# Performance work log

Hardware: AMD Instinct MI355X
Metric: run time of the kernel (lower is better)

Reference implementation:

```python
import jax, jax.numpy as jnp
import numpy as np

DIM, N_HEAD, DK, DV = 1024, 16, 64, 64
B, S = 1, 4096


def setup_inputs() -> dict:
    key = jax.random.key(0)
    ks = jax.random.split(key, 9)
    sd = 0.02
    return {
        "x": jax.random.normal(ks[0], (B, S, DIM), dtype=jnp.float32),
        "Wq": jax.random.normal(ks[1], (DIM, N_HEAD * DK), dtype=jnp.float32) * sd,
        "bq": jnp.zeros((N_HEAD * DK,), dtype=jnp.float32),
        "Wk": jax.random.normal(ks[2], (DIM, N_HEAD * DK), dtype=jnp.float32) * sd,
        "bk": jnp.zeros((N_HEAD * DK,), dtype=jnp.float32),
        "Wv": jax.random.normal(ks[3], (DIM, N_HEAD * DV), dtype=jnp.float32) * sd,
        "bv": jnp.zeros((N_HEAD * DV,), dtype=jnp.float32),
        "Wo": jax.random.normal(ks[4], (N_HEAD * DV, DIM), dtype=jnp.float32) * sd,
        "bo": jnp.zeros((DIM,), dtype=jnp.float32),
    }


def reference(x, Wq, bq, Wk, bk, Wv, bv, Wo, bo):
    b, s, _ = x.shape
    scale = DK ** (-0.5)
    # projections -> [b, h, s, d]
    q = (x @ Wq + bq).reshape(b, s, N_HEAD, DK).transpose(0, 2, 1, 3)
    k = (x @ Wk + bk).reshape(b, s, N_HEAD, DK).transpose(0, 2, 1, 3)
    v = (x @ Wv + bv).reshape(b, s, N_HEAD, DV).transpose(0, 2, 1, 3)
    attn = jnp.einsum("bhqd,bhkd->bhqk", q, k) * scale  # [b,h,s,s]
    attn = jax.nn.softmax(attn, axis=-1)
    out = jnp.einsum("bhqk,bhkd->bhqd", attn, v)  # [b,h,s,dv]
    out = out.transpose(0, 2, 1, 3).reshape(b, s, N_HEAD * DV)
    return out @ Wo + bo
```

## Files before the change

kernel.cpp:

```cpp
#include <hip/hip_runtime.h>
#include <hip/hip_bf16.h>
#include <hip/hip_fp16.h>

#define SEQ 4096
#define DIM 1024
#define NH 16
#define NT (SEQ / 64)

typedef __attribute__((ext_vector_type(4))) float f32x4;
typedef __attribute__((ext_vector_type(16))) float f32x16;
typedef __attribute__((ext_vector_type(8))) _Float16 half8;
typedef __attribute__((ext_vector_type(4))) _Float16 half4;

typedef const unsigned __attribute__((address_space(1)))* gas_t;
typedef unsigned __attribute__((address_space(3)))* las_t;

#if __has_builtin(__builtin_amdgcn_exp2f)
#define EXP2(x) __builtin_amdgcn_exp2f(x)
#else
#define EXP2(x) exp2f(x)
#endif

#define SMC 0.18033688f

__global__ __launch_bounds__(256) void prep_all(const float* __restrict__ x,
                                                _Float16* __restrict__ xh,
                                                const float* __restrict__ W0,
                                                const float* __restrict__ W1,
                                                const float* __restrict__ W2,
                                                const float* __restrict__ W3,
                                                _Float16* __restrict__ T0,
                                                _Float16* __restrict__ T1,
                                                _Float16* __restrict__ T2,
                                                _Float16* __restrict__ T3) {
  if (blockIdx.z == 4) {
    const int blkid = blockIdx.x * 32 + blockIdx.y;
#pragma unroll
    for (int u = 0; u < 4; u++) {
      int i = blkid * 4096 + u * 1024 + threadIdx.x * 4;
      float4 v = *reinterpret_cast<const float4*>(x + i);
      half4 h;
      h[0] = (_Float16)v.x; h[1] = (_Float16)v.y;
      h[2] = (_Float16)v.z; h[3] = (_Float16)v.w;
      *reinterpret_cast<half4*>(xh + i) = h;
    }
    return;
  }
  const float* W = blockIdx.z == 0 ? W0 : blockIdx.z == 1 ? W1 : blockIdx.z == 2 ? W2 : W3;
  _Float16* Wt = blockIdx.z == 0 ? T0 : blockIdx.z == 1 ? T1 : blockIdx.z == 2 ? T2 : T3;
  __shared__ float t[32][33];
  int bx = blockIdx.x * 32;
  int by = blockIdx.y * 32;
  int tx = threadIdx.x & 31, ty = threadIdx.x >> 5;
#pragma unroll
  for (int i = 0; i < 4; i++)
    t[ty + i * 8][tx] = W[(by + ty + i * 8) * DIM + bx + tx];
  __syncthreads();
#pragma unroll
  for (int i = 0; i < 4; i++)
    Wt[(bx + ty + i * 8) * DIM + by + tx] = (_Float16)t[tx][ty + i * 8];
}

template <int MODE>
__device__ __forceinline__ void gemm_body(const _Float16* __restrict__ A,
                                          const _Float16* __restrict__ Bt,
                                          const float* __restrict__ bias,
                                          void* __restrict__ outp,
                                          int M, int N, int Kd, int bmb, int bnb) {
  __shared__ __align__(16) _Float16 As[128][32];
  __shared__ __align__(16) _Float16 Bs[128][32];
  const int tid = threadIdx.x, lane = tid & 63, w = tid >> 6;
  const int bm = bmb * 128, bn = bnb * 128;
  const int l15 = lane & 15, g = lane >> 4, kb = g * 8;
  const int wr = (w >> 1) * 64, wc = (w & 1) * 64;
  const int lr = lane >> 2;
  const int lc = (lane & 3) * 8;
  f32x4 acc[4][4] = {};

  for (int k0 = 0; k0 < Kd; k0 += 32) {
    __syncthreads();
    const _Float16* as0 = A + (size_t)(bm + w * 32 + lr) * Kd + k0 + lc;
    __builtin_amdgcn_global_load_lds((gas_t)(const void*)as0,
                                     (las_t)(void*)&As[w * 32][0], 16, 0, 0);
    __builtin_amdgcn_global_load_lds((gas_t)(const void*)(as0 + (size_t)16 * Kd),
                                     (las_t)(void*)&As[w * 32 + 16][0], 16, 0, 0);
    const _Float16* bs0 = Bt + (size_t)(bn + w * 32 + lr) * Kd + k0 + lc;
    __builtin_amdgcn_global_load_lds((gas_t)(const void*)bs0,
                                     (las_t)(void*)&Bs[w * 32][0], 16, 0, 0);
    __builtin_amdgcn_global_load_lds((gas_t)(const void*)(bs0 + (size_t)16 * Kd),
                                     (las_t)(void*)&Bs[w * 32 + 16][0], 16, 0, 0);
    __syncthreads();

    half8 af[4], bf[4];
#pragma unroll
    for (int i = 0; i < 4; i++)
      af[i] = *reinterpret_cast<const half8*>(&As[wr + i * 16 + l15][kb]);
#pragma unroll
    for (int j = 0; j < 4; j++)
      bf[j] = *reinterpret_cast<const half8*>(&Bs[wc + j * 16 + l15][kb]);
    __builtin_amdgcn_s_setprio(1);
#pragma unroll
    for (int i = 0; i < 4; i++)
#pragma unroll
      for (int j = 0; j < 4; j++)
        acc[i][j] = __builtin_amdgcn_mfma_f32_16x16x32_f16(af[i], bf[j], acc[i][j], 0, 0, 0);
    __builtin_amdgcn_s_setprio(0);
  }

  const int gswap = ((g & 1) << 1) | (g >> 1);
#pragma unroll
  for (int i = 0; i < 4; i++)
#pragma unroll
    for (int j = 0; j < 4; j++) {
      const int col = bn + wc + j * 16 + l15;
      if (MODE == 2) {
        const int rowP = bm + wr + i * 16 + gswap * 4;
        half4 hv;
#pragma unroll
        for (int r = 0; r < 4; r++) hv[r] = (_Float16)(acc[i][j][r] + bias[col]);
        *reinterpret_cast<half4*>(&((_Float16*)outp)[(size_t)col * M + rowP]) = hv;
      } else {
        const int row0 = bm + wr + i * 16 + g * 4;
#pragma unroll
        for (int r = 0; r < 4; r++) {
          float vv = acc[i][j][r] + bias[col];
          if (MODE == 0) {
            _Float16* O = (_Float16*)outp;
            O[(((col >> 6) * SEQ) + row0 + r) * 64 + (col & 63)] = (_Float16)vv;
          } else {
            float* O = (float*)outp;
            O[(size_t)(row0 + r) * N + col] = vv;
          }
        }
      }
    }
}

__global__ __launch_bounds__(256) void gemm_qkv(const _Float16* __restrict__ A,
                                                const _Float16* __restrict__ WqT,
                                                const _Float16* __restrict__ WkT,
                                                const _Float16* __restrict__ WvT,
                                                const float* __restrict__ bq,
                                                const float* __restrict__ bk,
                                                const float* __restrict__ bv,
                                                _Float16* __restrict__ Qd,
                                                _Float16* __restrict__ Kd,
                                                _Float16* __restrict__ Vd) {
  if (blockIdx.z == 0)
    gemm_body<0>(A, WqT, bq, (void*)Qd, SEQ, DIM, DIM, blockIdx.x, blockIdx.y);
  else if (blockIdx.z == 1)
    gemm_body<0>(A, WkT, bk, (void*)Kd, SEQ, DIM, DIM, blockIdx.x, blockIdx.y);
  else
    gemm_body<2>(A, WvT, bv, (void*)Vd, SEQ, DIM, DIM, blockIdx.x, blockIdx.y);
}

__global__ __launch_bounds__(256) void gemm_out(const _Float16* __restrict__ A,
                                                const _Float16* __restrict__ Bt,
                                                const float* __restrict__ bias,
                                                float* __restrict__ out) {
  gemm_body<1>(A, Bt, bias, (void*)out, SEQ, DIM, DIM, blockIdx.x, blockIdx.y);
}

__global__ __launch_bounds__(512) void attn_fwd(const _Float16* __restrict__ Q,
                                                const _Float16* __restrict__ Kh,
                                                const _Float16* __restrict__ Vt_g,
                                                _Float16* __restrict__ Og) {
  __shared__ __align__(16) _Float16 Ks[3][64][72];
  __shared__ __align__(16) _Float16 Vs[3][64][72];
  const int hh = blockIdx.y;
  const int q0 = blockIdx.x * 256;
  const int tid = threadIdx.x, lane = tid & 63, w = tid >> 6;
  const int l31 = lane & 31, hq = lane >> 5, h8 = hq * 8;

  const int qrow = q0 + w * 32 + l31;
  const _Float16* qp = Q + ((size_t)hh * SEQ + qrow) * 64;
  half8 qf[4];
#pragma unroll
  for (int d = 0; d < 4; d++)
    qf[d] = *reinterpret_cast<const half8*>(qp + d * 16 + h8);

  f32x16 o[2] = {};
  float m = -1e30f, lsum = 0.f, negmC = 1e30f;
  const f32x16 kZero16 = {};

  const int srow = tid >> 3, sc8 = (tid & 7) * 8;
  const _Float16* kbase = Kh + (size_t)hh * SEQ * 64;
  const _Float16* vbase = Vt_g + (size_t)hh * 64 * SEQ;

  uint4 kr, vr;
  auto LOADKV = [&](int kt2) {
    kr = *reinterpret_cast<const uint4*>(kbase + (size_t)(kt2 * 64 + srow) * 64 + sc8);
    vr = *reinterpret_cast<const uint4*>(vbase + (size_t)srow * SEQ + kt2 * 64 + sc8);
  };
  auto STAGE = [&](int buf) {
    *reinterpret_cast<uint4*>(&Ks[buf][srow][sc8]) = kr;
    *reinterpret_cast<uint4*>(&Vs[buf][srow][sc8]) = vr;
  };

  auto QK = [&](int tile, f32x16 (&sf)[2]) {
    const int b = tile % 3;
    __builtin_amdgcn_s_setprio(1);
    {
      half8 kf0 = *reinterpret_cast<const half8*>(&Ks[b][l31][h8]);
      half8 kf1 = *reinterpret_cast<const half8*>(&Ks[b][32 + l31][h8]);
      sf[0] = __builtin_amdgcn_mfma_f32_32x32x16_f16(kf0, qf[0], kZero16, 0, 0, 0);
      sf[1] = __builtin_amdgcn_mfma_f32_32x32x16_f16(kf1, qf[0], kZero16, 0, 0, 0);
    }
#pragma unroll
    for (int d = 1; d < 4; d++) {
      half8 kf0 = *reinterpret_cast<const half8*>(&Ks[b][l31][d * 16 + h8]);
      half8 kf1 = *reinterpret_cast<const half8*>(&Ks[b][32 + l31][d * 16 + h8]);
      sf[0] = __builtin_amdgcn_mfma_f32_32x32x16_f16(kf0, qf[d], sf[0], 0, 0, 0);
      sf[1] = __builtin_amdgcn_mfma_f32_32x32x16_f16(kf1, qf[d], sf[1], 0, 0, 0);
    }
    __builtin_amdgcn_s_setprio(0);
  };

  auto ITER = [&](int t, f32x16 (&scur)[2], f32x16 (&snext)[2]) {
    if (t + 1 < NT) QK(t + 1, snext);
    if (t + 2 < NT) STAGE((t + 2) % 3);
    if (t + 3 < NT) LOADKV(t + 3);

    float t0 = fmaxf(fmaxf(scur[0][0], scur[0][1]), scur[0][2]);
    float t1 = fmaxf(fmaxf(scur[0][3], scur[0][4]), scur[0][5]);
    float t2 = fmaxf(fmaxf(scur[0][6], scur[0][7]), scur[0][8]);
    float t3 = fmaxf(fmaxf(scur[0][9], scur[0][10]), scur[0][11]);
    float t4 = fmaxf(fmaxf(scur[0][12], scur[0][13]), scur[0][14]);
    float t5 = fmaxf(fmaxf(scur[0][15], scur[1][0]), scur[1][1]);
    float t6 = fmaxf(fmaxf(scur[1][2], scur[1][3]), scur[1][4]);
    float t7 = fmaxf(fmaxf(scur[1][5], scur[1][6]), scur[1][7]);
    float t8 = fmaxf(fmaxf(scur[1][8], scur[1][9]), scur[1][10]);
    float t9 = fmaxf(fmaxf(scur[1][11], scur[1][12]), scur[1][13]);
    float ta = fmaxf(scur[1][14], scur[1][15]);
    float u0 = fmaxf(fmaxf(t0, t1), t2);
    float u1 = fmaxf(fmaxf(t3, t4), t5);
    float u2 = fmaxf(fmaxf(t6, t7), t8);
    float u3 = fmaxf(t9, ta);
    float pm = fmaxf(fmaxf(fmaxf(u0, u1), u2), u3);

    if (__any(pm > m + 64.f)) {
      pm = fmaxf(pm, __shfl_xor(pm, 32, 64));
      float mn = fmaxf(m, pm);
      float al = EXP2((m - mn) * SMC);
      m = mn;
      negmC = -mn * SMC;
      lsum *= al;
      o[0] *= al;
      o[1] *= al;
    }
    f32x16 pf0, pf1;
    float s0 = 0.f, s1 = 0.f, s2 = 0.f, s3 = 0.f;
#pragma unroll
    for (int r = 0; r < 16; r += 4) {
      float p0 = EXP2(fmaf(scur[0][r + 0], SMC, negmC));
      float p1 = EXP2(fmaf(scur[0][r + 1], SMC, negmC));
      float p2 = EXP2(fmaf(scur[0][r + 2], SMC, negmC));
      float p3 = EXP2(fmaf(scur[0][r + 3], SMC, negmC));
      pf0[r + 0] = p0; pf0[r + 1] = p1; pf0[r + 2] = p2; pf0[r + 3] = p3;
      s0 += p0; s1 += p1; s2 += p2; s3 += p3;
    }
#pragma unroll
    for (int r = 0; r < 16; r += 4) {
      float p0 = EXP2(fmaf(scur[1][r + 0], SMC, negmC));
      float p1 = EXP2(fmaf(scur[1][r + 1], SMC, negmC));
      float p2 = EXP2(fmaf(scur[1][r + 2], SMC, negmC));
      float p3 = EXP2(fmaf(scur[1][r + 3], SMC, negmC));
      pf1[r + 0] = p0; pf1[r + 1] = p1; pf1[r + 2] = p2; pf1[r + 3] = p3;
      s0 += p0; s1 += p1; s2 += p2; s3 += p3;
    }
    lsum += (s0 + s1) + (s2 + s3);

    half8 pb[4];
#pragma unroll
    for (int s = 0; s < 4; s++) {
      const int base = (s & 1) * 8;
      unsigned d0, d1, d2, d3;
      if (s < 2) {
        d0 = __builtin_bit_cast(unsigned, __builtin_amdgcn_cvt_pkrtz(pf0[base + 0], pf0[base + 1]));
        d1 = __builtin_bit_cast(unsigned, __builtin_amdgcn_cvt_pkrtz(pf0[base + 2], pf0[base + 3]));
        d2 = __builtin_bit_cast(unsigned, __builtin_amdgcn_cvt_pkrtz(pf0[base + 4], pf0[base + 5]));
        d3 = __builtin_bit_cast(unsigned, __builtin_amdgcn_cvt_pkrtz(pf0[base + 6], pf0[base + 7]));
      } else {
        d0 = __builtin_bit_cast(unsigned, __builtin_amdgcn_cvt_pkrtz(pf1[base + 0], pf1[base + 1]));
        d1 = __builtin_bit_cast(unsigned, __builtin_amdgcn_cvt_pkrtz(pf1[base + 2], pf1[base + 3]));
        d2 = __builtin_bit_cast(unsigned, __builtin_amdgcn_cvt_pkrtz(pf1[base + 4], pf1[base + 5]));
        d3 = __builtin_bit_cast(unsigned, __builtin_amdgcn_cvt_pkrtz(pf1[base + 6], pf1[base + 7]));
      }
      uint4 uu = {d0, d1, d2, d3};
      pb[s] = __builtin_bit_cast(half8, uu);
    }

    const int bv = t % 3;
    __builtin_amdgcn_s_setprio(1);
#pragma unroll
    for (int s = 0; s < 4; s++) {
      half8 va0 = *reinterpret_cast<const half8*>(&Vs[bv][l31][s * 16 + h8]);
      half8 va1 = *reinterpret_cast<const half8*>(&Vs[bv][32 + l31][s * 16 + h8]);
      o[0] = __builtin_amdgcn_mfma_f32_32x32x16_f16(va0, pb[s], o[0], 0, 0, 0);
      o[1] = __builtin_amdgcn_mfma_f32_32x32x16_f16(va1, pb[s], o[1], 0, 0, 0);
    }
    __builtin_amdgcn_s_setprio(0);

    __syncthreads();
  };

  LOADKV(0); STAGE(0);
  LOADKV(1); STAGE(1);
  LOADKV(2);
  __syncthreads();

  f32x16 sfA[2], sfB[2];
  QK(0, sfA);
  for (int t = 0; t < NT; t += 2) {
    ITER(t, sfA, sfB);
    ITER(t + 1, sfB, sfA);
  }

  float ls = lsum + __shfl_xor(lsum, 32, 64);
  float rinv = 1.f / ls;
#pragma unroll
  for (int tile = 0; tile < 2; tile++)
#pragma unroll
    for (int rg = 0; rg < 4; rg++) {
      half4 hv;
#pragma unroll
      for (int j = 0; j < 4; j++) hv[j] = (_Float16)(o[tile][rg * 4 + j] * rinv);
      const int dv = tile * 32 + rg * 8 + 4 * hq;
      *reinterpret_cast<half4*>(&Og[(size_t)qrow * DIM + hh * 64 + dv]) = hv;
    }
}


extern "C" void kernel_launch(void* const* d_in, const int* in_sizes, int n_in,
                              void* d_out, int out_size, void* d_ws, size_t ws_size,
                              hipStream_t stream) {
  const float* x  = (const float*)d_in[0];
  const float* Wq = (const float*)d_in[1];
  const float* bq = (const float*)d_in[2];
  const float* Wk = (const float*)d_in[3];
  const float* bk = (const float*)d_in[4];
  const float* Wv = (const float*)d_in[5];
  const float* bv = (const float*)d_in[6];
  const float* Wo = (const float*)d_in[7];
  const float* bo = (const float*)d_in[8];

  char* ws = (char*)d_ws;
  _Float16* xh  = (_Float16*)ws;
  _Float16* WqT = (_Float16*)(ws + (size_t)SEQ * DIM * 2);
  _Float16* WkT = WqT + DIM * DIM;
  _Float16* WvT = WkT + DIM * DIM;
  _Float16* WoT = WvT + DIM * DIM;
  _Float16* Qd  = WoT + DIM * DIM;
  _Float16* Kd  = Qd + (size_t)SEQ * DIM;
  _Float16* Vd  = Kd + (size_t)SEQ * DIM;
  _Float16* Od  = Vd + (size_t)SEQ * DIM;

  prep_all<<<dim3(32, 32, 5), 256, 0, stream>>>(x, xh, Wq, Wk, Wv, Wo,
                                                WqT, WkT, WvT, WoT);

  gemm_qkv<<<dim3(SEQ / 128, DIM / 128, 3), 256, 0, stream>>>(
      xh, WqT, WkT, WvT, bq, bk, bv, Qd, Kd, Vd);

  attn_fwd<<<dim3(SEQ / 256, NH), 512, 0, stream>>>(Qd, Kd, Vd, Od);

  gemm_out<<<dim3(SEQ / 128, DIM / 128), 256, 0, stream>>>(Od, WoT, bo, (float*)d_out);
}
```

Baseline: 162.9 us.

## Give each attention wave two 32-row query tiles, halve block threads

The attention kernel now runs 256 threads per block (4 waves), each wave handling 64 query rows as two 32-row sub-tiles that share the same K and V fragments read from LDS. Each thread loads twice as much K/V per stage to keep the 256-row block tile. This halves LDS fragment reads per unit of MFMA work and doubles independent MFMA chains per wave. The cost is roughly double the accumulator and score registers per thread, with launch_bounds(256,1) allowing more VGPRs but possibly lowering occupancy.

```diff
diff --git a/kernel.cpp b/kernel.cpp
--- a/kernel.cpp
+++ b/kernel.cpp
@@ -161,10 +161,10 @@
   gemm_body<1>(A, Bt, bias, (void*)out, SEQ, DIM, DIM, blockIdx.x, blockIdx.y);
 }
 
-__global__ __launch_bounds__(512) void attn_fwd(const _Float16* __restrict__ Q,
-                                                const _Float16* __restrict__ Kh,
-                                                const _Float16* __restrict__ Vt_g,
-                                                _Float16* __restrict__ Og) {
+__global__ __launch_bounds__(256, 1) void attn_fwd(const _Float16* __restrict__ Q,
+                                                   const _Float16* __restrict__ Kh,
+                                                   const _Float16* __restrict__ Vt_g,
+                                                   _Float16* __restrict__ Og) {
   __shared__ __align__(16) _Float16 Ks[3][64][72];
   __shared__ __align__(16) _Float16 Vs[3][64][72];
   const int hh = blockIdx.y;
@@ -172,122 +172,139 @@
   const int tid = threadIdx.x, lane = tid & 63, w = tid >> 6;
   const int l31 = lane & 31, hq = lane >> 5, h8 = hq * 8;
 
-  const int qrow = q0 + w * 32 + l31;
-  const _Float16* qp = Q + ((size_t)hh * SEQ + qrow) * 64;
-  half8 qf[4];
-#pragma unroll
-  for (int d = 0; d < 4; d++)
-    qf[d] = *reinterpret_cast<const half8*>(qp + d * 16 + h8);
-
-  f32x16 o[2] = {};
-  float m = -1e30f, lsum = 0.f, negmC = 1e30f;
+  const int qrow0 = q0 + w * 64 + l31;
+  const _Float16* qp0 = Q + ((size_t)hh * SEQ + qrow0) * 64;
+  half8 qf[2][4];
+#pragma unroll
+  for (int d = 0; d < 4; d++) {
+    qf[0][d] = *reinterpret_cast<const half8*>(qp0 + d * 16 + h8);
+    qf[1][d] = *reinterpret_cast<const half8*>(qp0 + 32 * 64 + d * 16 + h8);
+  }
+
+  f32x16 o[2][2] = {};
+  float m[2] = {-1e30f, -1e30f};
+  float lsum[2] = {0.f, 0.f};
+  float negmC[2] = {1e30f, 1e30f};
   const f32x16 kZero16 = {};
 
-  const int srow = tid >> 3, sc8 = (tid & 7) * 8;
+  const int srow = tid >> 2, scc = (tid & 3) * 16;
   const _Float16* kbase = Kh + (size_t)hh * SEQ * 64;
   const _Float16* vbase = Vt_g + (size_t)hh * 64 * SEQ;
 
-  uint4 kr, vr;
+  uint4 kr0, kr1, vr0, vr1;
   auto LOADKV = [&](int kt2) {
-    kr = *reinterpret_cast<const uint4*>(kbase + (size_t)(kt2 * 64 + srow) * 64 + sc8);
-    vr = *reinterpret_cast<const uint4*>(vbase + (size_t)srow * SEQ + kt2 * 64 + sc8);
+    const _Float16* kp = kbase + (size_t)(kt2 * 64 + srow) * 64 + scc;
+    kr0 = *reinterpret_cast<const uint4*>(kp);
+    kr1 = *reinterpret_cast<const uint4*>(kp + 8);
+    const _Float16* vp = vbase + (size_t)srow * SEQ + kt2 * 64 + scc;
+    vr0 = *reinterpret_cast<const uint4*>(vp);
+    vr1 = *reinterpret_cast<const uint4*>(vp + 8);
   };
   auto STAGE = [&](int buf) {
-    *reinterpret_cast<uint4*>(&Ks[buf][srow][sc8]) = kr;
-    *reinterpret_cast<uint4*>(&Vs[buf][srow][sc8]) = vr;
+    *reinterpret_cast<uint4*>(&Ks[buf][srow][scc]) = kr0;
+    *reinterpret_cast<uint4*>(&Ks[buf][srow][scc + 8]) = kr1;
+    *reinterpret_cast<uint4*>(&Vs[buf][srow][scc]) = vr0;
+    *reinterpret_cast<uint4*>(&Vs[buf][srow][scc + 8]) = vr1;
   };
 
-  auto QK = [&](int tile, f32x16 (&sf)[2]) {
+  auto QK = [&](int tile, f32x16 (&sf)[2][2]) {
     const int b = tile % 3;
     __builtin_amdgcn_s_setprio(1);
     {
       half8 kf0 = *reinterpret_cast<const half8*>(&Ks[b][l31][h8]);
       half8 kf1 = *reinterpret_cast<const half8*>(&Ks[b][32 + l31][h8]);
-      sf[0] = __builtin_amdgcn_mfma_f32_32x32x16_f16(kf0, qf[0], kZero16, 0, 0, 0);
-      sf[1] = __builtin_amdgcn_mfma_f32_32x32x16_f16(kf1, qf[0], kZero16, 0, 0, 0);
+      sf[0][0] = __builtin_amdgcn_mfma_f32_32x32x16_f16(kf0, qf[0][0], kZero16, 0, 0, 0);
+      sf[0][1] = __builtin_amdgcn_mfma_f32_32x32x16_f16(kf1, qf[0][0], kZero16, 0, 0, 0);
+      sf[1][0] = __builtin_amdgcn_mfma_f32_32x32x16_f16(kf0, qf[1][0], kZero16, 0, 0, 0);
+      sf[1][1] = __builtin_amdgcn_mfma_f32_32x32x16_f16(kf1, qf[1][0], kZero16, 0, 0, 0);
     }
 #pragma unroll
     for (int d = 1; d < 4; d++) {
       half8 kf0 = *reinterpret_cast<const half8*>(&Ks[b][l31][d * 16 + h8]);
       half8 kf1 = *reinterpret_cast<const half8*>(&Ks[b][32 + l31][d * 16 + h8]);
-      sf[0] = __builtin_amdgcn_mfma_f32_32x32x16_f16(kf0, qf[d], sf[0], 0, 0, 0);
-      sf[1] = __builtin_amdgcn_mfma_f32_32x32x16_f16(kf1, qf[d], sf[1], 0, 0, 0);
+      sf[0][0] = __builtin_amdgcn_mfma_f32_32x32x16_f16(kf0, qf[0][d], sf[0][0], 0, 0, 0);
+      sf[0][1] = __builtin_amdgcn_mfma_f32_32x32x16_f16(kf1, qf[0][d], sf[0][1], 0, 0, 0);
+      sf[1][0] = __builtin_amdgcn_mfma_f32_32x32x16_f16(kf0, qf[1][d], sf[1][0], 0, 0, 0);
+      sf[1][1] = __builtin_amdgcn_mfma_f32_32x32x16_f16(kf1, qf[1][d], sf[1][1], 0, 0, 0);
     }
     __builtin_amdgcn_s_setprio(0);
   };
 
-  auto ITER = [&](int t, f32x16 (&scur)[2], f32x16 (&snext)[2]) {
+  auto ITER = [&](int t, f32x16 (&scur)[2][2], f32x16 (&snext)[2][2]) {
     if (t + 1 < NT) QK(t + 1, snext);
     if (t + 2 < NT) STAGE((t + 2) % 3);
     if (t + 3 < NT) LOADKV(t + 3);
 
-    float t0 = fmaxf(fmaxf(scur[0][0], scur[0][1]), scur[0][2]);
-    float t1 = fmaxf(fmaxf(scur[0][3], scur[0][4]), scur[0][5]);
-    float t2 = fmaxf(fmaxf(scur[0][6], scur[0][7]), scur[0][8]);
-    float t3 = fmaxf(fmaxf(scur[0][9], scur[0][10]), scur[0][11]);
-    float t4 = fmaxf(fmaxf(scur[0][12], scur[0][13]), scur[0][14]);
-    float t5 = fmaxf(fmaxf(scur[0][15], scur[1][0]), scur[1][1]);
-    float t6 = fmaxf(fmaxf(scur[1][2], scur[1][3]), scur[1][4]);
-    float t7 = fmaxf(fmaxf(scur[1][5], scur[1][6]), scur[1][7]);
-    float t8 = fmaxf(fmaxf(scur[1][8], scur[1][9]), scur[1][10]);
-    float t9 = fmaxf(fmaxf(scur[1][11], scur[1][12]), scur[1][13]);
-    float ta = fmaxf(scur[1][14], scur[1][15]);
-    float u0 = fmaxf(fmaxf(t0, t1), t2);
-    float u1 = fmaxf(fmaxf(t3, t4), t5);
-    float u2 = fmaxf(fmaxf(t6, t7), t8);
-    float u3 = fmaxf(t9, ta);
-    float pm = fmaxf(fmaxf(fmaxf(u0, u1), u2), u3);
-
-    if (__any(pm > m + 64.f)) {
-      pm = fmaxf(pm, __shfl_xor(pm, 32, 64));
-      float mn = fmaxf(m, pm);
-      float al = EXP2((m - mn) * SMC);
-      m = mn;
-      negmC = -mn * SMC;
-      lsum *= al;
-      o[0] *= al;
-      o[1] *= al;
-    }
-    f32x16 pf0, pf1;
-    float s0 = 0.f, s1 = 0.f, s2 = 0.f, s3 = 0.f;
-#pragma unroll
-    for (int r = 0; r < 16; r += 4) {
-      float p0 = EXP2(fmaf(scur[0][r + 0], SMC, negmC));
-      float p1 = EXP2(fmaf(scur[0][r + 1], SMC, negmC));
-      float p2 = EXP2(fmaf(scur[0][r + 2], SMC, negmC));
-      float p3 = EXP2(fmaf(scur[0][r + 3], SMC, negmC));
-      pf0[r + 0] = p0; pf0[r + 1] = p1; pf0[r + 2] = p2; pf0[r + 3] = p3;
-      s0 += p0; s1 += p1; s2 += p2; s3 += p3;
-    }
-#pragma unroll
-    for (int r = 0; r < 16; r += 4) {
-      float p0 = EXP2(fmaf(scur[1][r + 0], SMC, negmC));
-      float p1 = EXP2(fmaf(scur[1][r + 1], SMC, negmC));
-      float p2 = EXP2(fmaf(scur[1][r + 2], SMC, negmC));
-      float p3 = EXP2(fmaf(scur[1][r + 3], SMC, negmC));
-      pf1[r + 0] = p0; pf1[r + 1] = p1; pf1[r + 2] = p2; pf1[r + 3] = p3;
-      s0 += p0; s1 += p1; s2 += p2; s3 += p3;
-    }
-    lsum += (s0 + s1) + (s2 + s3);
-
-    half8 pb[4];
-#pragma unroll
-    for (int s = 0; s < 4; s++) {
-      const int base = (s & 1) * 8;
-      unsigned d0, d1, d2, d3;
-      if (s < 2) {
-        d0 = __builtin_bit_cast(unsigned, __builtin_amdgcn_cvt_pkrtz(pf0[base + 0], pf0[base + 1]));
-        d1 = __builtin_bit_cast(unsigned, __builtin_amdgcn_cvt_pkrtz(pf0[base + 2], pf0[base + 3]));
-        d2 = __builtin_bit_cast(unsigned, __builtin_amdgcn_cvt_pkrtz(pf0[base + 4], pf0[base + 5]));
-        d3 = __builtin_bit_cast(unsigned, __builtin_amdgcn_cvt_pkrtz(pf0[base + 6], pf0[base + 7]));
-      } else {
-        d0 = __builtin_bit_cast(unsigned, __builtin_amdgcn_cvt_pkrtz(pf1[base + 0], pf1[base + 1]));
-        d1 = __builtin_bit_cast(unsigned, __builtin_amdgcn_cvt_pkrtz(pf1[base + 2], pf1[base + 3]));
-        d2 = __builtin_bit_cast(unsigned, __builtin_amdgcn_cvt_pkrtz(pf1[base + 4], pf1[base + 5]));
-        d3 = __builtin_bit_cast(unsigned, __builtin_amdgcn_cvt_pkrtz(pf1[base + 6], pf1[base + 7]));
-      }
-      uint4 uu = {d0, d1, d2, d3};
-      pb[s] = __builtin_bit_cast(half8, uu);
+    half8 pb[2][4];
+#pragma unroll
+    for (int qa = 0; qa < 2; qa++) {
+      float t0 = fmaxf(fmaxf(scur[qa][0][0], scur[qa][0][1]), scur[qa][0][2]);
+      float t1 = fmaxf(fmaxf(scur[qa][0][3], scur[qa][0][4]), scur[qa][0][5]);
+      float t2 = fmaxf(fmaxf(scur[qa][0][6], scur[qa][0][7]), scur[qa][0][8]);
+      float t3 = fmaxf(fmaxf(scur[qa][0][9], scur[qa][0][10]), scur[qa][0][11]);
+      float t4 = fmaxf(fmaxf(scur[qa][0][12], scur[qa][0][13]), scur[qa][0][14]);
+      float t5 = fmaxf(fmaxf(scur[qa][0][15], scur[qa][1][0]), scur[qa][1][1]);
+      float t6 = fmaxf(fmaxf(scur[qa][1][2], scur[qa][1][3]), scur[qa][1][4]);
+      float t7 = fmaxf(fmaxf(scur[qa][1][5], scur[qa][1][6]), scur[qa][1][7]);
+      float t8 = fmaxf(fmaxf(scur[qa][1][8], scur[qa][1][9]), scur[qa][1][10]);
+      float t9 = fmaxf(fmaxf(scur[qa][1][11], scur[qa][1][12]), scur[qa][1][13]);
+      float ta = fmaxf(scur[qa][1][14], scur[qa][1][15]);
+      float u0 = fmaxf(fmaxf(t0, t1), t2);
+      float u1 = fmaxf(fmaxf(t3, t4), t5);
+      float u2 = fmaxf(fmaxf(t6, t7), t8);
+      float u3 = fmaxf(t9, ta);
+      float pm = fmaxf(fmaxf(fmaxf(u0, u1), u2), u3);
+
+      if (__any(pm > m[qa] + 64.f)) {
+        pm = fmaxf(pm, __shfl_xor(pm, 32, 64));
+        float mn = fmaxf(m[qa], pm);
+        float al = EXP2((m[qa] - mn) * SMC);
+        m[qa] = mn;
+        negmC[qa] = -mn * SMC;
+        lsum[qa] *= al;
+        o[qa][0] *= al;
+        o[qa][1] *= al;
+      }
+      f32x16 pf0, pf1;
+      float s0 = 0.f, s1 = 0.f, s2 = 0.f, s3 = 0.f;
+#pragma unroll
+      for (int r = 0; r < 16; r += 4) {
+        float p0 = EXP2(fmaf(scur[qa][0][r + 0], SMC, negmC[qa]));
+        float p1 = EXP2(fmaf(scur[qa][0][r + 1], SMC, negmC[qa]));
+        float p2 = EXP2(fmaf(scur[qa][0][r + 2], SMC, negmC[qa]));
+        float p3 = EXP2(fmaf(scur[qa][0][r + 3], SMC, negmC[qa]));
+        pf0[r + 0] = p0; pf0[r + 1] = p1; pf0[r + 2] = p2; pf0[r + 3] = p3;
+        s0 += p0; s1 += p1; s2 += p2; s3 += p3;
+      }
+#pragma unroll
+      for (int r = 0; r < 16; r += 4) {
+        float p0 = EXP2(fmaf(scur[qa][1][r + 0], SMC, negmC[qa]));
+        float p1 = EXP2(fmaf(scur[qa][1][r + 1], SMC, negmC[qa]));
+        float p2 = EXP2(fmaf(scur[qa][1][r + 2], SMC, negmC[qa]));
+        float p3 = EXP2(fmaf(scur[qa][1][r + 3], SMC, negmC[qa]));
+        pf1[r + 0] = p0; pf1[r + 1] = p1; pf1[r + 2] = p2; pf1[r + 3] = p3;
+        s0 += p0; s1 += p1; s2 += p2; s3 += p3;
+      }
+      lsum[qa] += (s0 + s1) + (s2 + s3);
+
+#pragma unroll
+      for (int s = 0; s < 4; s++) {
+        const int base = (s & 1) * 8;
+        unsigned d0, d1, d2, d3;
+        if (s < 2) {
+          d0 = __builtin_bit_cast(unsigned, __builtin_amdgcn_cvt_pkrtz(pf0[base + 0], pf0[base + 1]));
+          d1 = __builtin_bit_cast(unsigned, __builtin_amdgcn_cvt_pkrtz(pf0[base + 2], pf0[base + 3]));
+          d2 = __builtin_bit_cast(unsigned, __builtin_amdgcn_cvt_pkrtz(pf0[base + 4], pf0[base + 5]));
+          d3 = __builtin_bit_cast(unsigned, __builtin_amdgcn_cvt_pkrtz(pf0[base + 6], pf0[base + 7]));
+        } else {
+          d0 = __builtin_bit_cast(unsigned, __builtin_amdgcn_cvt_pkrtz(pf1[base + 0], pf1[base + 1]));
+          d1 = __builtin_bit_cast(unsigned, __builtin_amdgcn_cvt_pkrtz(pf1[base + 2], pf1[base + 3]));
+          d2 = __builtin_bit_cast(unsigned, __builtin_amdgcn_cvt_pkrtz(pf1[base + 4], pf1[base + 5]));
+          d3 = __builtin_bit_cast(unsigned, __builtin_amdgcn_cvt_pkrtz(pf1[base + 6], pf1[base + 7]));
+        }
+        uint4 uu = {d0, d1, d2, d3};
+        pb[qa][s] = __builtin_bit_cast(half8, uu);
+      }
     }
 
     const int bv = t % 3;
@@ -296,8 +313,10 @@
     for (int s = 0; s < 4; s++) {
       half8 va0 = *reinterpret_cast<const half8*>(&Vs[bv][l31][s * 16 + h8]);
       half8 va1 = *reinterpret_cast<const half8*>(&Vs[bv][32 + l31][s * 16 + h8]);
-      o[0] = __builtin_amdgcn_mfma_f32_32x32x16_f16(va0, pb[s], o[0], 0, 0, 0);
-      o[1] = __builtin_amdgcn_mfma_f32_32x32x16_f16(va1, pb[s], o[1], 0, 0, 0);
+      o[0][0] = __builtin_amdgcn_mfma_f32_32x32x16_f16(va0, pb[0][s], o[0][0], 0, 0, 0);
+      o[0][1] = __builtin_amdgcn_mfma_f32_32x32x16_f16(va1, pb[0][s], o[0][1], 0, 0, 0);
+      o[1][0] = __builtin_amdgcn_mfma_f32_32x32x16_f16(va0, pb[1][s], o[1][0], 0, 0, 0);
+      o[1][1] = __builtin_amdgcn_mfma_f32_32x32x16_f16(va1, pb[1][s], o[1][1], 0, 0, 0);
     }
     __builtin_amdgcn_s_setprio(0);
 
@@ -309,25 +328,29 @@
   LOADKV(2);
   __syncthreads();
 
-  f32x16 sfA[2], sfB[2];
+  f32x16 sfA[2][2], sfB[2][2];
   QK(0, sfA);
   for (int t = 0; t < NT; t += 2) {
     ITER(t, sfA, sfB);
     ITER(t + 1, sfB, sfA);
   }
 
-  float ls = lsum + __shfl_xor(lsum, 32, 64);
-  float rinv = 1.f / ls;
-#pragma unroll
-  for (int tile = 0; tile < 2; tile++)
-#pragma unroll
-    for (int rg = 0; rg < 4; rg++) {
-      half4 hv;
-#pragma unroll
-      for (int j = 0; j < 4; j++) hv[j] = (_Float16)(o[tile][rg * 4 + j] * rinv);
-      const int dv = tile * 32 + rg * 8 + 4 * hq;
-      *reinterpret_cast<half4*>(&Og[(size_t)qrow * DIM + hh * 64 + dv]) = hv;
-    }
+#pragma unroll
+  for (int qa = 0; qa < 2; qa++) {
+    float ls = lsum[qa] + __shfl_xor(lsum[qa], 32, 64);
+    float rinv = 1.f / ls;
+    const size_t orow = (size_t)(qrow0 + 32 * qa) * DIM + hh * 64;
+#pragma unroll
+    for (int tile = 0; tile < 2; tile++)
+#pragma unroll
+      for (int rg = 0; rg < 4; rg++) {
+        half4 hv;
+#pragma unroll
+        for (int j = 0; j < 4; j++) hv[j] = (_Float16)(o[qa][tile][rg * 4 + j] * rinv);
+        const int dv = tile * 32 + rg * 8 + 4 * hq;
+        *reinterpret_cast<half4*>(&Og[orow + dv]) = hv;
+      }
+  }
 }
 
 
@@ -361,7 +384,7 @@
   gemm_qkv<<<dim3(SEQ / 128, DIM / 128, 3), 256, 0, stream>>>(
       xh, WqT, WkT, WvT, bq, bk, bv, Qd, Kd, Vd);
 
-  attn_fwd<<<dim3(SEQ / 256, NH), 512, 0, stream>>>(Qd, Kd, Vd, Od);
+  attn_fwd<<<dim3(SEQ / 256, NH), 256, 0, stream>>>(Qd, Kd, Vd, Od);
 
   gemm_out<<<dim3(SEQ / 128, DIM / 128), 256, 0, stream>>>(Od, WoT, bo, (float*)d_out);
 }
```

New measurement: 183.7 us. 1.13x slower.
